# Optimization experiments

Measured on AMD Instinct MI355X. Metric: run time of the kernel, lower is better.

Reference implementation:

```python
import jax, jax.numpy as jnp
import numpy as np

B = 2048          # graphs in dense batch
NPG = 64          # nodes per graph (molecules are small)
N = B * NPG       # 131072 total nodes
E = 524288        # directed edges, avg degree 4
D = 275           # dim_inner
L = 5             # layers_mp
NF = 9            # atom categorical features
V = 128           # per-feature vocab
BN_EPS = 1e-5


def setup_inputs() -> dict:
    key = jax.random.key(0)
    ks = jax.random.split(key, 8)
    return {
        "x_atoms": jax.random.randint(ks[0], (N, NF), 0, 119, dtype=jnp.int64),
        "edge_index": jax.random.randint(ks[1], (2, E), 0, N, dtype=jnp.int64),
        "atom_emb": jax.random.normal(ks[2], (NF, V, D), jnp.float32) * 0.1,
        "conv_W": jax.random.normal(ks[3], (L, D, D), jnp.float32) * (1.0 / np.sqrt(D)),
        "conv_b": jnp.zeros((L, D), jnp.float32),
        "bn_gamma": jnp.ones((L, D), jnp.float32),
        "bn_beta": jnp.zeros((L, D), jnp.float32),
        "post_W": jax.random.normal(ks[4], (D, D), jnp.float32) * (1.0 / np.sqrt(D)),
        "post_b": jnp.zeros((D,), jnp.float32),
    }


def reference(x_atoms, edge_index, atom_emb, conv_W, conv_b, bn_gamma, bn_beta, post_W, post_b):
    n = x_atoms.shape[0]
    # AtomEncoder: sum of per-feature embedding lookups -> [N, D]
    h = jax.vmap(lambda tab, idx: tab[idx], in_axes=(0, 1))(atom_emb, x_atoms).sum(0)

    # GCN normalization with self loops (shared across layers since graph is fixed)
    loops = jnp.arange(n, dtype=edge_index.dtype)
    row = jnp.concatenate([edge_index[0], loops])  # source
    col = jnp.concatenate([edge_index[1], loops])  # target (aggregation index)
    deg = jax.ops.segment_sum(jnp.ones_like(row, h.dtype), col, num_segments=n)
    dinv = jnp.where(deg > 0, jax.lax.rsqrt(jnp.maximum(deg, 1e-12)), 0.0)
    norm = dinv[row] * dinv[col]  # [E+N]

    for i in range(L):
        xw = h @ conv_W[i].T                                   # [N, D] linear (no bias yet)
        msg = norm[:, None] * xw[row]                          # gather + edge scaling
        agg = jax.ops.segment_sum(msg, col, num_segments=n) + conv_b[i]
        # BatchNorm1d (training-mode batch stats, biased variance)
        mu = agg.mean(axis=0)
        var = agg.var(axis=0)
        hbn = (agg - mu) * jax.lax.rsqrt(var + BN_EPS) * bn_gamma[i] + bn_beta[i]
        h = jax.nn.relu(hbn)

    # post_mp: single Linear (MLPNoAct, num_layers=1)
    h = h @ post_W.T + post_b

    # graph_preprocess -> dense batch [B, NPG, D], then pairwise dot-product decode
    hd = h.reshape(B, NPG, D)
    logits = jnp.einsum('bnd,bmd->bnm', hd, hd)[..., None]     # [B, NPG, NPG, 1]
    return logits
```

## Files before the change

### kernel.cpp

```cpp
#include <hip/hip_runtime.h>
#include <hip/hip_bf16.h>
#include <cstdint>

#define NN 131072
#define NE 524288
#define DIM 275
#define DP 288
#define NFEAT 9
#define NVOC 128
#define NLAY 5
#define NPG 64
#define NGRAPH 2048
#define BN_EPS 1e-5f
#define BK 32
#define NEPAD (NE + 3 * NN)
#define LDSE 1536

typedef unsigned short u16;
typedef __attribute__((ext_vector_type(8))) short s16x8;
typedef __attribute__((ext_vector_type(4))) float f32x4;

__device__ __forceinline__ float bf2f(u16 u) {
  union { unsigned int i; float f; } x; x.i = ((unsigned int)u) << 16; return x.f;
}
__device__ __forceinline__ u16 f2bf(float f) {
  union { float f; unsigned int i; } x; x.f = f;
  unsigned int r = x.i + 0x7fffu + ((x.i >> 16) & 1u);
  return (u16)(r >> 16);
}
__device__ __forceinline__ void acc4(float* a, uint2 m) {
  a[0] += bf2f((u16)m.x); a[1] += bf2f((u16)(m.x >> 16));
  a[2] += bf2f((u16)m.y); a[3] += bf2f((u16)(m.y >> 16));
}


__global__ void hist_kernel(const int* __restrict__ ei, int* __restrict__ cnt) {
  int e = blockIdx.x * 256 + threadIdx.x;
  if (e < NE) atomicAdd(&cnt[ei[NE + e]], 1);
}

__global__ void pad_dinv_kernel(const int* __restrict__ cnt, int* __restrict__ cnt_pad,
                                float* __restrict__ dinv) {
  int v = blockIdx.x * 256 + threadIdx.x;
  if (v < NN) {
    int c = cnt[v];
    cnt_pad[v] = (c + 3) & ~3;
    dinv[v] = rsqrtf(1.0f + (float)c);
  }
}

__global__ void scan_block_kernel(const int* __restrict__ in, int* __restrict__ out_ex,
                                  int* __restrict__ partials) {
  __shared__ int buf[2][1024];
  int t = threadIdx.x;
  int idx = blockIdx.x * 1024 + t;
  int v = in[idx];
  buf[0][t] = v;
  __syncthreads();
  int cur = 0;
  for (int off = 1; off < 1024; off <<= 1) {
    int x = buf[cur][t];
    if (t >= off) x += buf[cur][t - off];
    buf[cur ^ 1][t] = x;
    __syncthreads();
    cur ^= 1;
  }
  out_ex[idx] = buf[cur][t] - v;
  if (t == 1023) partials[blockIdx.x] = buf[cur][t];
}

__global__ void scan_partials_kernel(int* partials) {
  __shared__ int buf[2][128];
  int t = threadIdx.x;
  int v = partials[t];
  buf[0][t] = v;
  __syncthreads();
  int cur = 0;
  for (int off = 1; off < 128; off <<= 1) {
    int x = buf[cur][t];
    if (t >= off) x += buf[cur][t - off];
    buf[cur ^ 1][t] = x;
    __syncthreads();
    cur ^= 1;
  }
  partials[t] = buf[cur][t] - v;
}

__global__ void add_offsets_kernel(int* __restrict__ indptr, const int* __restrict__ partials,
                                   int* __restrict__ cursor, const int* __restrict__ cnt_pad) {
  int i = blockIdx.x * 256 + threadIdx.x;
  if (i < NN) {
    int v = indptr[i] + partials[i >> 10];
    indptr[i] = v;
    cursor[i] = v;
    if (i == NN - 1) indptr[NN] = v + cnt_pad[NN - 1];
  }
}

__global__ void fill_csr_kernel(const int* __restrict__ ei, int* __restrict__ cursor,
                                int* __restrict__ srcs) {
  int e = blockIdx.x * 256 + threadIdx.x;
  if (e < NE) {
    int c = ei[NE + e];
    int p = atomicAdd(&cursor[c], 1);
    srcs[p] = ei[e];
  }
}

__global__ void pad_fill_kernel(const int* __restrict__ cursor, const int* __restrict__ indptr,
                                int* __restrict__ srcs) {
  int v = blockIdx.x * 256 + threadIdx.x;
  if (v < NN) {
    int pe = indptr[v + 1];
    for (int p = cursor[v]; p < pe; ++p) srcs[p] = NN;
  }
}

__global__ void zrow_kernel(u16* __restrict__ P, u16* __restrict__ Q) {
  int i = threadIdx.x;
  if (i < DP) {
    P[(size_t)NN * DP + i] = 0;
    Q[(size_t)NN * DP + i] = 0;
  }
}

__global__ void wpad_kernel(const float* __restrict__ convW, const float* __restrict__ postW,
                            u16* __restrict__ Wp) {
  int i = blockIdx.x * 256 + threadIdx.x;
  const int total = 6 * 320 * DP;
  if (i >= total) return;
  int k = i % DP;
  int r = i / DP;
  int j = r % 320;
  int m = r / 320;
  float val = 0.f;
  if (j < DIM && k < DIM)
    val = (m < 5) ? convW[((size_t)m * DIM + j) * DIM + k] : postW[(size_t)j * DIM + k];
  Wp[i] = f2bf(val);
}


__global__ void embed_kernel(const int* __restrict__ xa, const float* __restrict__ emb,
                             u16* __restrict__ P) {
  int n = blockIdx.x;
  int idx[NFEAT];
#pragma unroll
  for (int f = 0; f < NFEAT; ++f) idx[f] = xa[n * NFEAT + f];
  for (int d = threadIdx.x; d < DP; d += 128) {
    float s = 0.f;
    if (d < DIM) {
#pragma unroll
      for (int f = 0; f < NFEAT; ++f) s += emb[((size_t)f * NVOC + idx[f]) * DIM + d];
    }
    P[(size_t)n * DP + d] = f2bf(s);
  }
}


__device__ __forceinline__ uint4 xform8(uint4 r, const float* __restrict__ sc,
                                        const float* __restrict__ sh, int k) {
  union { uint4 u; u16 h[8]; } in, out;
  in.u = r;
#pragma unroll
  for (int j = 0; j < 8; ++j) {
    float x = fmaf(bf2f(in.h[j]), sc[k + j], sh[k + j]);
    out.h[j] = f2bf(fmaxf(x, 0.f));
  }
  return out.u;
}

__launch_bounds__(256)
__global__ void gemm_kernel(const u16* __restrict__ A, const u16* __restrict__ Wp,
                            u16* __restrict__ C,
                            const float* __restrict__ scale, const float* __restrict__ shift,
                            const float* __restrict__ rowscale, const float* __restrict__ colbias) {
  __shared__ __align__(16) u16 Bs[2][320 * 40];
  const int tid = threadIdx.x, lane = tid & 63, wv = tid >> 6;
  const int lr = lane & 15, lk = lane >> 4;
  const int row0 = blockIdx.x * 128 + wv * 32;
  const u16* ag0 = A + (size_t)(row0 + lr) * DP + lk * 8;
  const u16* ag1 = ag0 + (size_t)16 * DP;
  const int srow = tid >> 2, schk = tid & 3;
  const u16* sg = Wp + (size_t)srow * DP + schk * 8;
  const int swoff = srow * 40 + schk * 8;
  const int bbase = lr * 40 + lk * 8;
  const bool bn = (scale != nullptr);

#pragma unroll
  for (int i = 0; i < 5; ++i) {
    uint4 rb = *(const uint4*)(sg + (size_t)(64 * i) * DP);
    *(uint4*)&Bs[0][swoff + 64 * i * 40] = rb;
  }
  uint4 a0 = *(const uint4*)(ag0);
  uint4 a1 = *(const uint4*)(ag1);
  __syncthreads();

  f32x4 acc0[18], acc1[18];
#pragma unroll
  for (int j = 0; j < 18; ++j) {
    acc0[j] = (f32x4){0.f, 0.f, 0.f, 0.f};
    acc1[j] = (f32x4){0.f, 0.f, 0.f, 0.f};
  }

#pragma unroll 1
  for (int s = 0; s < 9; ++s) {
    const bool more = (s < 8);
    uint4 n0, n1, nb0, nb1, nb2, nb3, nb4;
    if (more) {
      int k = (s + 1) * BK;
      nb0 = *(const uint4*)(sg + k);
      nb1 = *(const uint4*)(sg + (size_t)64 * DP + k);
      nb2 = *(const uint4*)(sg + (size_t)128 * DP + k);
      nb3 = *(const uint4*)(sg + (size_t)192 * DP + k);
      nb4 = *(const uint4*)(sg + (size_t)256 * DP + k);
      n0 = *(const uint4*)(ag0 + k);
      n1 = *(const uint4*)(ag1 + k);
    }
    if (bn) {
      int kk = s * BK + lk * 8;
      a0 = xform8(a0, scale, shift, kk);
      a1 = xform8(a1, scale, shift, kk);
    }
    union { uint4 u; s16x8 v; } ca, cb;
    ca.u = a0; s16x8 af0 = ca.v;
    cb.u = a1; s16x8 af1 = cb.v;
    const u16* bp = &Bs[s & 1][bbase];
#pragma unroll
    for (int j = 0; j < 18; ++j) {
      s16x8 bf = *(const s16x8*)&bp[j * 640];
      acc0[j] = __builtin_amdgcn_mfma_f32_16x16x32_bf16(af0, bf, acc0[j], 0, 0, 0);
      acc1[j] = __builtin_amdgcn_mfma_f32_16x16x32_bf16(af1, bf, acc1[j], 0, 0, 0);
    }
    if (more) {
      u16* bq = &Bs[(s + 1) & 1][swoff];
      *(uint4*)&bq[0] = nb0;
      *(uint4*)&bq[64 * 40] = nb1;
      *(uint4*)&bq[128 * 40] = nb2;
      *(uint4*)&bq[192 * 40] = nb3;
      *(uint4*)&bq[256 * 40] = nb4;
      a0 = n0; a1 = n1;
    }
    __syncthreads();
  }

#pragma unroll
  for (int i = 0; i < 2; ++i) {
    int gr0 = row0 + i * 16 + lk * 4;
    float rs[4];
#pragma unroll
    for (int r = 0; r < 4; ++r) rs[r] = rowscale ? rowscale[gr0 + r] : 1.f;
#pragma unroll
    for (int j = 0; j < 18; ++j) {
      f32x4 av = i ? acc1[j] : acc0[j];
      int gc = j * 16 + lr;
      float cb = (colbias && gc < DIM) ? colbias[gc] : 0.f;
#pragma unroll
      for (int r = 0; r < 4; ++r) {
        u16 o = (gc < DIM) ? f2bf(fmaf(av[r], rs[r], cb)) : (u16)0;
        C[(size_t)(gr0 + r) * DP + gc] = o;
      }
    }
  }
}


__launch_bounds__(256)
__global__ void spmm_kernel(const u16* __restrict__ X, u16* __restrict__ Y,
                            const int* __restrict__ indptr, const int* __restrict__ srcs,
                            const float* __restrict__ dinv, const float* __restrict__ bias,
                            float* __restrict__ bn_sum, float* __restrict__ bn_sq) {
  __shared__ float ls[DP], lq[DP];
  __shared__ int sptr[65];
  __shared__ int sidx[LDSE];
  int tid = threadIdx.x;
  for (int i = tid; i < DP; i += 256) { ls[i] = 0.f; lq[i] = 0.f; }
  int vb = blockIdx.x * 64;
  if (tid < 65) sptr[tid] = indptr[vb + tid];
  __syncthreads();
  int ebase = sptr[0];
  int ecnt = sptr[64] - ebase;
  const int* ip;
  if (ecnt <= LDSE) {
    for (int i = tid; i < ecnt; i += 256) sidx[i] = srcs[ebase + i];
    ip = sidx;
  } else {
    ip = srcs + ebase;
  }
  __syncthreads();

  int lane = tid & 63, wv = tid >> 6;
  int c0 = lane << 2;
  int c1 = 256 + (lane << 2);
  bool tl = lane < 8;
  float bia[4], bib[4];
#pragma unroll
  for (int j = 0; j < 4; ++j) bia[j] = bias[c0 + j];
#pragma unroll
  for (int j = 0; j < 4; ++j) bib[j] = (tl && c1 + j < DIM) ? bias[c1 + j] : 0.f;
  float s0[4] = {}, q0[4] = {}, s1[4] = {}, q1[4] = {};

  for (int g = 0; g < 8; ++g) {
    int nA = wv * 16 + g;
    int nB = nA + 8;
    int ebA = sptr[nA] - ebase, neA = sptr[nA + 1] - sptr[nA];
    int ebB = sptr[nB] - ebase, neB = sptr[nB + 1] - sptr[nB];
    int nemax = neA > neB ? neA : neB;
    const u16* xA = X + (size_t)(vb + nA) * DP;
    const u16* xB = X + (size_t)(vb + nB) * DP;
    uint2 mA = *(const uint2*)(xA + c0);
    uint2 mB = *(const uint2*)(xB + c0);
    uint2 tA, tB;
    if (tl) { tA = *(const uint2*)(xA + c1); tB = *(const uint2*)(xB + c1); }
    float A0[4] = {}, B0[4] = {}, A1[4] = {}, B1[4] = {};
    acc4(A0, mA); acc4(B0, mB);
    if (tl) { acc4(A1, tA); acc4(B1, tB); }

    for (int e = 0; e < nemax; e += 4) {
      bool aA = e < neA, aB = e < neB;
      int oA = aA ? ebA + e : 0;
      int oB = aB ? ebB + e : 0;
      int ia[4], ib[4];
#pragma unroll
      for (int j = 0; j < 4; ++j) {
        int va = ip[oA + j], vbx = ip[oB + j];
        ia[j] = aA ? va : NN;
        ib[j] = aB ? vbx : NN;
      }
      const u16* pa[4]; const u16* pb[4];
#pragma unroll
      for (int j = 0; j < 4; ++j) {
        pa[j] = X + (size_t)ia[j] * DP;
        pb[j] = X + (size_t)ib[j] * DP;
      }
      uint2 ma[4], mb[4];
#pragma unroll
      for (int j = 0; j < 4; ++j) ma[j] = *(const uint2*)(pa[j] + c0);
#pragma unroll
      for (int j = 0; j < 4; ++j) mb[j] = *(const uint2*)(pb[j] + c0);
      uint2 ta[4], tb[4];
      if (tl) {
#pragma unroll
        for (int j = 0; j < 4; ++j) ta[j] = *(const uint2*)(pa[j] + c1);
#pragma unroll
        for (int j = 0; j < 4; ++j) tb[j] = *(const uint2*)(pb[j] + c1);
      }
#pragma unroll
      for (int j = 0; j < 4; ++j) { acc4(A0, ma[j]); acc4(B0, mb[j]); }
      if (tl) {
#pragma unroll
        for (int j = 0; j < 4; ++j) { acc4(A1, ta[j]); acc4(B1, tb[j]); }
      }
    }

    float dvA = dinv[vb + nA], dvB = dinv[vb + nB];
    u16* yA = Y + (size_t)(vb + nA) * DP;
    u16* yB = Y + (size_t)(vb + nB) * DP;
    float ya[4], yb[4];
#pragma unroll
    for (int j = 0; j < 4; ++j) {
      ya[j] = fmaf(dvA, A0[j], bia[j]);
      s0[j] += ya[j]; q0[j] += ya[j] * ya[j];
      yb[j] = fmaf(dvB, B0[j], bia[j]);
      s0[j] += yb[j]; q0[j] += yb[j] * yb[j];
    }
    uint2 wa, wb;
    wa.x = (unsigned)f2bf(ya[0]) | ((unsigned)f2bf(ya[1]) << 16);
    wa.y = (unsigned)f2bf(ya[2]) | ((unsigned)f2bf(ya[3]) << 16);
    wb.x = (unsigned)f2bf(yb[0]) | ((unsigned)f2bf(yb[1]) << 16);
    wb.y = (unsigned)f2bf(yb[2]) | ((unsigned)f2bf(yb[3]) << 16);
    *(uint2*)(yA + c0) = wa;
    *(uint2*)(yB + c0) = wb;
    if (tl) {
      float za[4], zb[4];
#pragma unroll
      for (int j = 0; j < 4; ++j) {
        za[j] = fmaf(dvA, A1[j], bib[j]);
        s1[j] += za[j]; q1[j] += za[j] * za[j];
        zb[j] = fmaf(dvB, B1[j], bib[j]);
        s1[j] += zb[j]; q1[j] += zb[j] * zb[j];
      }
      uint2 ua, ub;
      ua.x = (unsigned)f2bf(za[0]) | ((unsigned)f2bf(za[1]) << 16);
      ua.y = (unsigned)f2bf(za[2]) | ((unsigned)f2bf(za[3]) << 16);
      ub.x = (unsigned)f2bf(zb[0]) | ((unsigned)f2bf(zb[1]) << 16);
      ub.y = (unsigned)f2bf(zb[2]) | ((unsigned)f2bf(zb[3]) << 16);
      *(uint2*)(yA + c1) = ua;
      *(uint2*)(yB + c1) = ub;
    }
  }

#pragma unroll
  for (int j = 0; j < 4; ++j) { atomicAdd(&ls[c0 + j], s0[j]); atomicAdd(&lq[c0 + j], q0[j]); }
  if (tl) {
#pragma unroll
    for (int j = 0; j < 4; ++j) { atomicAdd(&ls[c1 + j], s1[j]); atomicAdd(&lq[c1 + j], q1[j]); }
  }
  __syncthreads();
  for (int i = tid; i < DP; i += 256) {
    atomicAdd(&bn_sum[i], ls[i]);
    atomicAdd(&bn_sq[i], lq[i]);
  }
}

__global__ void bn_finalize_kernel(const float* __restrict__ bn_sum, const float* __restrict__ bn_sq,
                                   const float* __restrict__ gamma, const float* __restrict__ beta,
                                   float* __restrict__ scale, float* __restrict__ shift) {
  int d = threadIdx.x;
  if (d >= DP) return;
  if (d < DIM) {
    const float invN = 1.0f / (float)NN;
    float mu = bn_sum[d] * invN;
    float var = bn_sq[d] * invN - mu * mu;
    float rstd = rsqrtf(var + BN_EPS);
    float sc = gamma[d] * rstd;
    scale[d] = sc;
    shift[d] = fmaf(-mu, sc, beta[d]);
  } else {
    scale[d] = 0.f;
    shift[d] = 0.f;
  }
}


__launch_bounds__(256)
__global__ void decode_kernel(const u16* __restrict__ H, float* __restrict__ out) {
  __shared__ __align__(16) u16 tile[4][2][NPG * BK];
  int tid = threadIdx.x, lane = tid & 63, wv = tid >> 6;
  int g = blockIdx.x * 4 + wv;
  const u16* Hg = H + (size_t)g * NPG * DP;
  const int ssl = lane & 3;
  int soff[4];
  const u16* sg[4];
#pragma unroll
  for (int i = 0; i < 4; ++i) {
    int r = (lane >> 2) + i * 16;
    soff[i] = r * BK + ((ssl ^ (r & 3) ^ ((r >> 2) & 3)) << 3);
    sg[i] = Hg + (size_t)r * DP + ssl * 8;
  }
  const int fr = lane & 15, fs = lane >> 4;
  const int fswz = ((fs ^ (fr & 3) ^ ((fr >> 2) & 3)) << 3);
  int foff[4];
#pragma unroll
  for (int i = 0; i < 4; ++i) foff[i] = (i * 16 + fr) * BK + fswz;

  u16* t0 = tile[wv][0];
  u16* t1 = tile[wv][1];
  uint4 rg[4];
#pragma unroll
  for (int i = 0; i < 4; ++i) rg[i] = *(const uint4*)(sg[i]);
#pragma unroll
  for (int i = 0; i < 4; ++i) *(uint4*)&t0[soff[i]] = rg[i];

  f32x4 acc[4][4];
#pragma unroll
  for (int i = 0; i < 4; ++i)
#pragma unroll
    for (int j = 0; j < 4; ++j) acc[i][j] = (f32x4){0.f, 0.f, 0.f, 0.f};

  for (int s = 0; s < DP / BK; ++s) {
    u16* cur = (s & 1) ? t1 : t0;
    u16* nxt = (s & 1) ? t0 : t1;
    const bool more = (s < DP / BK - 1);
    if (more) {
#pragma unroll
      for (int i = 0; i < 4; ++i) rg[i] = *(const uint4*)(sg[i] + (s + 1) * BK);
    }
    s16x8 af[4];
#pragma unroll
    for (int i = 0; i < 4; ++i) af[i] = *(const s16x8*)&cur[foff[i]];
#pragma unroll
    for (int i = 0; i < 4; ++i)
#pragma unroll
      for (int j = 0; j < 4; ++j)
        acc[i][j] = __builtin_amdgcn_mfma_f32_16x16x32_bf16(af[i], af[j], acc[i][j], 0, 0, 0);
    if (more) {
#pragma unroll
      for (int i = 0; i < 4; ++i) *(uint4*)&nxt[soff[i]] = rg[i];
    }
  }
  float* og = out + (size_t)g * NPG * NPG;
#pragma unroll
  for (int i = 0; i < 4; ++i) {
    int m0 = i * 16 + fs * 4;
#pragma unroll
    for (int j = 0; j < 4; ++j) {
      int n = j * 16 + fr;
#pragma unroll
      for (int r = 0; r < 4; ++r) og[(m0 + r) * NPG + n] = acc[i][j][r];
    }
  }
}


extern "C" void kernel_launch(void* const* d_in, const int* in_sizes, int n_in,
                              void* d_out, int out_size, void* d_ws, size_t ws_size,
                              hipStream_t stream) {
  const int* xa = (const int*)d_in[0];
  const int* ei = (const int*)d_in[1];
  const float* emb = (const float*)d_in[2];
  const float* convW = (const float*)d_in[3];
  const float* convB = (const float*)d_in[4];
  const float* gamma = (const float*)d_in[5];
  const float* beta = (const float*)d_in[6];
  const float* postW = (const float*)d_in[7];
  const float* postB = (const float*)d_in[8];
  float* out = (float*)d_out;

  char* w = (char*)d_ws;
  u16* P = (u16*)w;          w += (size_t)(NN + 1) * DP * sizeof(u16);
  u16* Q = (u16*)w;          w += (size_t)(NN + 1) * DP * sizeof(u16);
  u16* Wp = (u16*)w;         w += (size_t)6 * 320 * DP * sizeof(u16);
  float* dinv = (float*)w;   w += (size_t)NN * sizeof(float);
  int* cnt = (int*)w;        w += (size_t)NN * sizeof(int);
  int* cnt_pad = (int*)w;    w += (size_t)NN * sizeof(int);
  int* indptr = (int*)w;     w += (size_t)(NN + 64) * sizeof(int);
  int* cursor = (int*)w;     w += (size_t)NN * sizeof(int);
  int* srcs = (int*)w;       w += (size_t)NEPAD * sizeof(int);
  int* partials = (int*)w;   w += 256 * sizeof(int);
  float* bn_sum = (float*)w; w += DP * sizeof(float);
  float* bn_sq = (float*)w;  w += DP * sizeof(float);
  float* bnscale = (float*)w; w += DP * sizeof(float);
  float* bnshift = (float*)w; w += DP * sizeof(float);

  size_t need = (size_t)(w - (char*)d_ws);
  if (ws_size < need) return;

  hipMemsetAsync(cnt, 0, (size_t)NN * sizeof(int), stream);
  hist_kernel<<<NE / 256, 256, 0, stream>>>(ei, cnt);
  pad_dinv_kernel<<<NN / 256, 256, 0, stream>>>(cnt, cnt_pad, dinv);
  scan_block_kernel<<<NN / 1024, 1024, 0, stream>>>(cnt_pad, indptr, partials);
  scan_partials_kernel<<<1, 128, 0, stream>>>(partials);
  add_offsets_kernel<<<NN / 256, 256, 0, stream>>>(indptr, partials, cursor, cnt_pad);
  fill_csr_kernel<<<NE / 256, 256, 0, stream>>>(ei, cursor, srcs);
  pad_fill_kernel<<<NN / 256, 256, 0, stream>>>(cursor, indptr, srcs);
  wpad_kernel<<<(6 * 320 * DP + 255) / 256, 256, 0, stream>>>(convW, postW, Wp);
  embed_kernel<<<NN, 128, 0, stream>>>(xa, emb, P);
  zrow_kernel<<<1, 288, 0, stream>>>(P, Q);

  for (int l = 0; l < NLAY; ++l) {
    gemm_kernel<<<NN / 128, 256, 0, stream>>>(
        P, Wp + (size_t)l * 320 * DP, Q,
        l ? bnscale : nullptr, l ? bnshift : nullptr, dinv, nullptr);
    hipMemsetAsync(bn_sum, 0, 2 * DP * sizeof(float), stream);
    spmm_kernel<<<NN / 64, 256, 0, stream>>>(Q, P, indptr, srcs, dinv,
                                             convB + (size_t)l * DIM, bn_sum, bn_sq);
    bn_finalize_kernel<<<1, DP, 0, stream>>>(bn_sum, bn_sq, gamma + (size_t)l * DIM,
                                             beta + (size_t)l * DIM, bnscale, bnshift);
  }

  gemm_kernel<<<NN / 128, 256, 0, stream>>>(
      P, Wp + (size_t)5 * 320 * DP, Q, bnscale, bnshift, nullptr, postB);

  decode_kernel<<<NGRAPH / 4, 256, 0, stream>>>(Q, out);
}
```

Baseline: 1.217 ms.

## Retile GEMM to 64-row LDS-staged A tiles and fold BN finalize into GEMM

The GEMM now stages both the A and W tiles through swizzled shared memory, using 64-row blocks split 2x2 across waves, where it previously held A in registers with 128-row blocks. The BN affine transform is applied once per element when a tile is written to LDS, rather than redundantly in each wave's registers. The separate bn_finalize kernel and the per-layer memset are removed: each GEMM block computes scale and shift from the raw statistics, which are kept in one buffer per layer and zeroed once up front. The cost is a single LDS buffer with two barriers per k-step, which loses the previous double buffering, and roughly twice as many W tile loads in total.

```diff
diff --git a/kernel.cpp b/kernel.cpp
--- a/kernel.cpp
+++ b/kernel.cpp
@@ -157,8 +157,8 @@
 }
 
 
-__device__ __forceinline__ uint4 xform8(uint4 r, const float* __restrict__ sc,
-                                        const float* __restrict__ sh, int k) {
+__device__ __forceinline__ uint4 xform8s(uint4 r, const float* __restrict__ sc,
+                                         const float* __restrict__ sh, int k) {
   union { uint4 u; u16 h[8]; } in, out;
   in.u = r;
 #pragma unroll
@@ -172,32 +172,74 @@
 __launch_bounds__(256)
 __global__ void gemm_kernel(const u16* __restrict__ A, const u16* __restrict__ Wp,
                             u16* __restrict__ C,
-                            const float* __restrict__ scale, const float* __restrict__ shift,
+                            const float* __restrict__ bn_sum, const float* __restrict__ bn_sq,
+                            const float* __restrict__ gamma, const float* __restrict__ beta,
                             const float* __restrict__ rowscale, const float* __restrict__ colbias) {
-  __shared__ __align__(16) u16 Bs[2][320 * 40];
+  __shared__ __align__(16) u16 Asl[64 * BK];
+  __shared__ __align__(16) u16 Bsl[288 * BK];
+  __shared__ float scs[DP], shs[DP];
   const int tid = threadIdx.x, lane = tid & 63, wv = tid >> 6;
-  const int lr = lane & 15, lk = lane >> 4;
-  const int row0 = blockIdx.x * 128 + wv * 32;
-  const u16* ag0 = A + (size_t)(row0 + lr) * DP + lk * 8;
-  const u16* ag1 = ag0 + (size_t)16 * DP;
+  const int wm = wv & 1, wn = wv >> 1;
+  const int row0 = blockIdx.x * 64;
+  const bool bn = (bn_sum != nullptr);
+
+  for (int d = tid; d < DP; d += 256) {
+    float sc = 1.f, sh = 0.f;
+    if (bn) {
+      if (d < DIM) {
+        const float invN = 1.0f / (float)NN;
+        float mu = bn_sum[d] * invN;
+        float var = bn_sq[d] * invN - mu * mu;
+        float rstd = rsqrtf(var + BN_EPS);
+        sc = gamma[d] * rstd;
+        sh = fmaf(-mu, sc, beta[d]);
+      } else {
+        sc = 0.f; sh = 0.f;
+      }
+    }
+    scs[d] = sc; shs[d] = sh;
+  }
+
   const int srow = tid >> 2, schk = tid & 3;
-  const u16* sg = Wp + (size_t)srow * DP + schk * 8;
-  const int swoff = srow * 40 + schk * 8;
-  const int bbase = lr * 40 + lk * 8;
-  const bool bn = (scale != nullptr);
-
-#pragma unroll
-  for (int i = 0; i < 5; ++i) {
-    uint4 rb = *(const uint4*)(sg + (size_t)(64 * i) * DP);
-    *(uint4*)&Bs[0][swoff + 64 * i * 40] = rb;
-  }
-  uint4 a0 = *(const uint4*)(ag0);
-  uint4 a1 = *(const uint4*)(ag1);
-  __syncthreads();
-
-  f32x4 acc0[18], acc1[18];
-#pragma unroll
-  for (int j = 0; j < 18; ++j) {
+  const int swz = ((schk ^ (srow & 3) ^ ((srow >> 2) & 3)) << 3);
+  const int awoff = srow * BK + swz;
+  const u16* ag = A + (size_t)(row0 + srow) * DP + schk * 8;
+  const u16* bg = Wp + (size_t)srow * DP + schk * 8;
+  const bool st4 = (tid < 128);
+
+  const int fr = lane & 15, fs = lane >> 4;
+  int aoff[2], boff[9];
+#pragma unroll
+  for (int i = 0; i < 2; ++i) {
+    int r = wm * 32 + i * 16 + fr;
+    aoff[i] = r * BK + ((fs ^ (r & 3) ^ ((r >> 2) & 3)) << 3);
+  }
+#pragma unroll
+  for (int j = 0; j < 9; ++j) {
+    int r = wn * 144 + j * 16 + fr;
+    boff[j] = r * BK + ((fs ^ (r & 3) ^ ((r >> 2) & 3)) << 3);
+  }
+
+  uint4 ra = *(const uint4*)(ag);
+  uint4 rb0 = *(const uint4*)(bg);
+  uint4 rb1 = *(const uint4*)(bg + (size_t)64 * DP);
+  uint4 rb2 = *(const uint4*)(bg + (size_t)128 * DP);
+  uint4 rb3 = *(const uint4*)(bg + (size_t)192 * DP);
+  uint4 rb4;
+  if (st4) rb4 = *(const uint4*)(bg + (size_t)256 * DP);
+  __syncthreads();
+  if (bn) ra = xform8s(ra, scs, shs, schk * 8);
+  *(uint4*)&Asl[awoff] = ra;
+  *(uint4*)&Bsl[awoff] = rb0;
+  *(uint4*)&Bsl[awoff + 64 * BK] = rb1;
+  *(uint4*)&Bsl[awoff + 128 * BK] = rb2;
+  *(uint4*)&Bsl[awoff + 192 * BK] = rb3;
+  if (st4) *(uint4*)&Bsl[awoff + 256 * BK] = rb4;
+  __syncthreads();
+
+  f32x4 acc0[9], acc1[9];
+#pragma unroll
+  for (int j = 0; j < 9; ++j) {
     acc0[j] = (f32x4){0.f, 0.f, 0.f, 0.f};
     acc1[j] = (f32x4){0.f, 0.f, 0.f, 0.f};
   }
@@ -205,54 +247,47 @@
 #pragma unroll 1
   for (int s = 0; s < 9; ++s) {
     const bool more = (s < 8);
-    uint4 n0, n1, nb0, nb1, nb2, nb3, nb4;
+    uint4 na, nb0, nb1, nb2, nb3, nb4;
     if (more) {
       int k = (s + 1) * BK;
-      nb0 = *(const uint4*)(sg + k);
-      nb1 = *(const uint4*)(sg + (size_t)64 * DP + k);
-      nb2 = *(const uint4*)(sg + (size_t)128 * DP + k);
-      nb3 = *(const uint4*)(sg + (size_t)192 * DP + k);
-      nb4 = *(const uint4*)(sg + (size_t)256 * DP + k);
-      n0 = *(const uint4*)(ag0 + k);
-      n1 = *(const uint4*)(ag1 + k);
-    }
-    if (bn) {
-      int kk = s * BK + lk * 8;
-      a0 = xform8(a0, scale, shift, kk);
-      a1 = xform8(a1, scale, shift, kk);
-    }
-    union { uint4 u; s16x8 v; } ca, cb;
-    ca.u = a0; s16x8 af0 = ca.v;
-    cb.u = a1; s16x8 af1 = cb.v;
-    const u16* bp = &Bs[s & 1][bbase];
-#pragma unroll
-    for (int j = 0; j < 18; ++j) {
-      s16x8 bf = *(const s16x8*)&bp[j * 640];
+      na = *(const uint4*)(ag + k);
+      nb0 = *(const uint4*)(bg + k);
+      nb1 = *(const uint4*)(bg + (size_t)64 * DP + k);
+      nb2 = *(const uint4*)(bg + (size_t)128 * DP + k);
+      nb3 = *(const uint4*)(bg + (size_t)192 * DP + k);
+      if (st4) nb4 = *(const uint4*)(bg + (size_t)256 * DP + k);
+    }
+    s16x8 af0 = *(const s16x8*)&Asl[aoff[0]];
+    s16x8 af1 = *(const s16x8*)&Asl[aoff[1]];
+#pragma unroll
+    for (int j = 0; j < 9; ++j) {
+      s16x8 bf = *(const s16x8*)&Bsl[boff[j]];
       acc0[j] = __builtin_amdgcn_mfma_f32_16x16x32_bf16(af0, bf, acc0[j], 0, 0, 0);
       acc1[j] = __builtin_amdgcn_mfma_f32_16x16x32_bf16(af1, bf, acc1[j], 0, 0, 0);
     }
+    __syncthreads();
     if (more) {
-      u16* bq = &Bs[(s + 1) & 1][swoff];
-      *(uint4*)&bq[0] = nb0;
-      *(uint4*)&bq[64 * 40] = nb1;
-      *(uint4*)&bq[128 * 40] = nb2;
-      *(uint4*)&bq[192 * 40] = nb3;
-      *(uint4*)&bq[256 * 40] = nb4;
-      a0 = n0; a1 = n1;
-    }
-    __syncthreads();
+      if (bn) na = xform8s(na, scs, shs, (s + 1) * BK + schk * 8);
+      *(uint4*)&Asl[awoff] = na;
+      *(uint4*)&Bsl[awoff] = nb0;
+      *(uint4*)&Bsl[awoff + 64 * BK] = nb1;
+      *(uint4*)&Bsl[awoff + 128 * BK] = nb2;
+      *(uint4*)&Bsl[awoff + 192 * BK] = nb3;
+      if (st4) *(uint4*)&Bsl[awoff + 256 * BK] = nb4;
+      __syncthreads();
+    }
   }
 
 #pragma unroll
   for (int i = 0; i < 2; ++i) {
-    int gr0 = row0 + i * 16 + lk * 4;
+    int gr0 = row0 + wm * 32 + i * 16 + fs * 4;
     float rs[4];
 #pragma unroll
     for (int r = 0; r < 4; ++r) rs[r] = rowscale ? rowscale[gr0 + r] : 1.f;
 #pragma unroll
-    for (int j = 0; j < 18; ++j) {
+    for (int j = 0; j < 9; ++j) {
       f32x4 av = i ? acc1[j] : acc0[j];
-      int gc = j * 16 + lr;
+      int gc = wn * 144 + j * 16 + fr;
       float cb = (colbias && gc < DIM) ? colbias[gc] : 0.f;
 #pragma unroll
       for (int r = 0; r < 4; ++r) {
@@ -402,25 +437,6 @@
   }
 }
 
-__global__ void bn_finalize_kernel(const float* __restrict__ bn_sum, const float* __restrict__ bn_sq,
-                                   const float* __restrict__ gamma, const float* __restrict__ beta,
-                                   float* __restrict__ scale, float* __restrict__ shift) {
-  int d = threadIdx.x;
-  if (d >= DP) return;
-  if (d < DIM) {
-    const float invN = 1.0f / (float)NN;
-    float mu = bn_sum[d] * invN;
-    float var = bn_sq[d] * invN - mu * mu;
-    float rstd = rsqrtf(var + BN_EPS);
-    float sc = gamma[d] * rstd;
-    scale[d] = sc;
-    shift[d] = fmaf(-mu, sc, beta[d]);
-  } else {
-    scale[d] = 0.f;
-    shift[d] = 0.f;
-  }
-}
-
 
 __launch_bounds__(256)
 __global__ void decode_kernel(const u16* __restrict__ H, float* __restrict__ out) {
@@ -517,15 +533,13 @@
   int* cursor = (int*)w;     w += (size_t)NN * sizeof(int);
   int* srcs = (int*)w;       w += (size_t)NEPAD * sizeof(int);
   int* partials = (int*)w;   w += 256 * sizeof(int);
-  float* bn_sum = (float*)w; w += DP * sizeof(float);
-  float* bn_sq = (float*)w;  w += DP * sizeof(float);
-  float* bnscale = (float*)w; w += DP * sizeof(float);
-  float* bnshift = (float*)w; w += DP * sizeof(float);
+  float* bnstats = (float*)w; w += (size_t)NLAY * 2 * DP * sizeof(float);
 
   size_t need = (size_t)(w - (char*)d_ws);
   if (ws_size < need) return;
 
   hipMemsetAsync(cnt, 0, (size_t)NN * sizeof(int), stream);
+  hipMemsetAsync(bnstats, 0, (size_t)NLAY * 2 * DP * sizeof(float), stream);
   hist_kernel<<<NE / 256, 256, 0, stream>>>(ei, cnt);
   pad_dinv_kernel<<<NN / 256, 256, 0, stream>>>(cnt, cnt_pad, dinv);
   scan_block_kernel<<<NN / 1024, 1024, 0, stream>>>(cnt_pad, indptr, partials);
@@ -538,18 +552,23 @@
   zrow_kernel<<<1, 288, 0, stream>>>(P, Q);
 
   for (int l = 0; l < NLAY; ++l) {
-    gemm_kernel<<<NN / 128, 256, 0, stream>>>(
+    const float* bs = l ? bnstats + (size_t)(l - 1) * 2 * DP : nullptr;
+    gemm_kernel<<<NN / 64, 256, 0, stream>>>(
         P, Wp + (size_t)l * 320 * DP, Q,
-        l ? bnscale : nullptr, l ? bnshift : nullptr, dinv, nullptr);
-    hipMemsetAsync(bn_sum, 0, 2 * DP * sizeof(float), stream);
+        bs, bs ? bs + DP : nullptr,
+        l ? gamma + (size_t)(l - 1) * DIM : nullptr,
+        l ? beta + (size_t)(l - 1) * DIM : nullptr,
+        dinv, nullptr);
     spmm_kernel<<<NN / 64, 256, 0, stream>>>(Q, P, indptr, srcs, dinv,
-                                             convB + (size_t)l * DIM, bn_sum, bn_sq);
-    bn_finalize_kernel<<<1, DP, 0, stream>>>(bn_sum, bn_sq, gamma + (size_t)l * DIM,
-                                             beta + (size_t)l * DIM, bnscale, bnshift);
-  }
-
-  gemm_kernel<<<NN / 128, 256, 0, stream>>>(
-      P, Wp + (size_t)5 * 320 * DP, Q, bnscale, bnshift, nullptr, postB);
+                                             convB + (size_t)l * DIM,
+                                             bnstats + (size_t)l * 2 * DP,
+                                             bnstats + (size_t)l * 2 * DP + DP);
+  }
+
+  const float* bs5 = bnstats + (size_t)4 * 2 * DP;
+  gemm_kernel<<<NN / 64, 256, 0, stream>>>(
+      P, Wp + (size_t)5 * 320 * DP, Q, bs5, bs5 + DP,
+      gamma + (size_t)4 * DIM, beta + (size_t)4 * DIM, nullptr, postB);
 
   decode_kernel<<<NGRAPH / 4, 256, 0, stream>>>(Q, out);
 }
```

Measured after the change: 1.030 ms. 1.18x faster.
